# Kernel optimization log

Hardware: AMD Instinct MI355X
Metric: run time of the kernel (lower is better)

## Reference

```python
import jax, jax.numpy as jnp
import numpy as np
import math

DIM = 1024
N_HEADS = 16
HEAD_DIM = DIM // N_HEADS
MAX_LEN = 4096
THETA = 10000.0
LN_EPS = 1e-5


def _rope_tables(dim, max_len, theta=THETA):
    # matches precompute_rope: freqs over even indices, angles = outer(t, freqs)
    inv = 1.0 / theta ** (np.arange(0, dim, 2, dtype=np.float32) / dim)
    t = np.arange(max_len, dtype=np.float32)
    ang = np.outer(t, inv)  # [max_len, dim//2]
    return jnp.asarray(np.cos(ang)), jnp.asarray(np.sin(ang))


def setup_inputs() -> dict:
    key = jax.random.key(0)
    ks = jax.random.split(key, 5)
    B, T, D = 2, 2048, DIM
    s = 1.0 / math.sqrt(D)
    x = jax.random.normal(ks[0], (B, T, D), dtype=jnp.float32)
    wq = jax.random.normal(ks[1], (D, D), dtype=jnp.float32) * s
    wk = jax.random.normal(ks[2], (D, D), dtype=jnp.float32) * s
    wv = jax.random.normal(ks[3], (D, D), dtype=jnp.float32) * s
    wo = jax.random.normal(ks[4], (D, D), dtype=jnp.float32) * s
    ln_g = jnp.ones((D,), dtype=jnp.float32)
    ln_b = jnp.zeros((D,), dtype=jnp.float32)
    cos, sin = _rope_tables(HEAD_DIM, MAX_LEN)
    return {"x": x, "wq": wq, "wk": wk, "wv": wv, "wo": wo,
            "ln_g": ln_g, "ln_b": ln_b, "cos": cos, "sin": sin}


def _rotate(x, cos, sin):
    # x: [B, T, H, hd]; complex multiply on interleaved (even, odd) pairs
    B, T, H, hd = x.shape
    xr = x.reshape(B, T, H, hd // 2, 2)
    x0, x1 = xr[..., 0], xr[..., 1]
    c = cos[None, :T, None, :]
    s = sin[None, :T, None, :]
    o0 = x0 * c - x1 * s
    o1 = x0 * s + x1 * c
    return jnp.stack([o0, o1], axis=-1).reshape(B, T, H, hd)


def reference(x, wq, wk, wv, wo, ln_g, ln_b, cos, sin):
    B, T, D = x.shape
    H, hd = N_HEADS, HEAD_DIM
    # LayerNorm
    mu = jnp.mean(x, axis=-1, keepdims=True)
    var = jnp.var(x, axis=-1, keepdims=True)
    h = (x - mu) * jax.lax.rsqrt(var + LN_EPS) * ln_g + ln_b
    # QKV projections (torch Linear: h @ W.T)
    q = jnp.einsum('btd,ed->bte', h, wq).reshape(B, T, H, hd)
    k = jnp.einsum('btd,ed->bte', h, wk).reshape(B, T, H, hd)
    v = jnp.einsum('btd,ed->bte', h, wv).reshape(B, T, H, hd)
    q = _rotate(q, cos, sin)
    k = _rotate(k, cos, sin)
    # full (non-causal) attention, scores [B, H, T, T]
    scores = jnp.einsum('bqhd,bkhd->bhqk', q, k) / math.sqrt(hd)
    attn = jax.nn.softmax(scores, axis=-1)
    out = jnp.einsum('bhqk,bkhd->bqhd', attn, v).reshape(B, T, D)
    return jnp.einsum('btd,ed->bte', out, wo)
```

## Files before the change

kernel.cpp:

```cpp
#include <hip/hip_runtime.h>
#include <hip/hip_bf16.h>

typedef __attribute__((ext_vector_type(4))) float          fx4;
typedef __attribute__((ext_vector_type(8))) __bf16         bfx8;
typedef __attribute__((ext_vector_type(8))) unsigned short usx8;
typedef __attribute__((ext_vector_type(4))) unsigned short usx4;

#define TLEN 2048
#define ROWS 4096
#define D    1024

__device__ __forceinline__ float bf2f(unsigned short u) {
    union { unsigned int i; float f; } v; v.i = ((unsigned int)u) << 16; return v.f;
}
__device__ __forceinline__ unsigned short f2bf(float f) {
    union { float f; unsigned int i; } v; v.f = f;
    unsigned int r = v.i + 0x7fffu + ((v.i >> 16) & 1u);
    return (unsigned short)(r >> 16);
}
__device__ __forceinline__ unsigned int cvtpk_bf16(float lo, float hi) {
    unsigned int r;
    asm("v_cvt_pk_bf16_f32 %0, %1, %2" : "=v"(r) : "v"(lo), "v"(hi));
    return r;
}
__device__ __forceinline__ void gload_lds16(const unsigned short* g, unsigned short* l) {
    __builtin_amdgcn_global_load_lds((const __attribute__((address_space(1))) void*)g,
                                     (__attribute__((address_space(3))) void*)l, 16, 0, 0);
}

__device__ __forceinline__ usx4 cvt4(fx4 a) {
    usx4 o;
    #pragma unroll
    for (int j = 0; j < 4; j++) o[j] = f2bf(a[j]);
    return o;
}
__global__ __launch_bounds__(256) void prep_kernel(const float* __restrict__ x,
                                                   const float* __restrict__ g,
                                                   const float* __restrict__ bta,
                                                   const float* __restrict__ wq, const float* __restrict__ wk,
                                                   const float* __restrict__ wv, const float* __restrict__ wo,
                                                   unsigned short* __restrict__ hout,
                                                   unsigned short* __restrict__ wqkv,
                                                   unsigned short* __restrict__ wob,
                                                   float* __restrict__ ropeTab) {
    const int tid = threadIdx.x;
    if (blockIdx.x >= 5120) {
        const int idx = (blockIdx.x - 5120) * 256 + tid;
        const int pi_ = idx >> 11, t = idx & 2047;
        float inv = __builtin_amdgcn_exp2f(-0.415241011861f * (float)pi_);
        float ang = (float)t * inv;
        ropeTab[idx * 2]     = cosf(ang);
        ropeTab[idx * 2 + 1] = sinf(ang);
        return;
    }
    if (blockIdx.x >= 4096) {
        const int i = (blockIdx.x - 4096) * 256 + tid;
        ((usx4*)wqkv)[i]          = cvt4(((const fx4*)wq)[i]);
        ((usx4*)wqkv)[262144 + i] = cvt4(((const fx4*)wk)[i]);
        ((usx4*)wqkv)[524288 + i] = cvt4(((const fx4*)wv)[i]);
        ((usx4*)wob)[i]           = cvt4(((const fx4*)wo)[i]);
        return;
    }
    const int row = blockIdx.x;
    fx4 v = ((const fx4*)(x + (size_t)row * D))[tid];
    float s  = v[0] + v[1] + v[2] + v[3];
    float s2 = v[0]*v[0] + v[1]*v[1] + v[2]*v[2] + v[3]*v[3];
    #pragma unroll
    for (int mk = 32; mk >= 1; mk >>= 1) { s += __shfl_xor(s, mk); s2 += __shfl_xor(s2, mk); }
    __shared__ float red[8];
    const int wave = tid >> 6, lane = tid & 63;
    if (lane == 0) { red[wave] = s; red[4 + wave] = s2; }
    __syncthreads();
    s  = red[0] + red[1] + red[2] + red[3];
    s2 = red[4] + red[5] + red[6] + red[7];
    float mu   = s * (1.0f / D);
    float var  = s2 * (1.0f / D) - mu * mu;
    float rstd = rsqrtf(var + 1e-5f);
    fx4 gv = ((const fx4*)g)[tid];
    fx4 bv = ((const fx4*)bta)[tid];
    usx4 o;
    #pragma unroll
    for (int j = 0; j < 4; j++) o[j] = f2bf((v[j] - mu) * rstd * gv[j] + bv[j]);
    ((usx4*)hout)[(size_t)row * 256 + tid] = o;
}

__global__ __launch_bounds__(512) void qkvt_gemm(const unsigned short* __restrict__ hbuf,
                                                 const unsigned short* __restrict__ wqkv,
                                                 unsigned short* __restrict__ qkout,
                                                 unsigned short* __restrict__ vtout,
                                                 const float* __restrict__ ropeTab) {
    constexpr int K = 1024;
    __shared__ __align__(16) unsigned short As[2][256 * 64];
    __shared__ __align__(16) unsigned short Bs[2][256 * 64];
    const int tid = threadIdx.x, lane = tid & 63, wave = tid >> 6;
    const int fr = lane & 15, fq = lane >> 4;
    const int wr = wave >> 2, wc = wave & 3;

    const int id = blockIdx.x;
    const bool isqk = id < 128;
    int bm, bn;
    const unsigned short *Ab, *Bb;
    if (isqk) {
        bm = id & 15; bn = id >> 4;
        Ab = hbuf + (size_t)(bm * 256) * K;
        Bb = wqkv + (size_t)(bn * 256) * K;
    } else {
        int j = id - 128; bm = j & 3; bn = j >> 2;
        Ab = wqkv + (size_t)(2048 * 1024) + (size_t)(bm * 256) * K;
        Bb = hbuf + (size_t)(bn * 256) * K;
    }

    const int srow   = wave * 8 + (lane >> 3);
    const int sc_dst = (lane & 7) * 8;
    const int sc_src = ((lane & 7) ^ (lane >> 3)) * 8;

    #define STAGE_Q(BUF, KT)                                                          \
        {                                                                             \
            _Pragma("unroll")                                                         \
            for (int i = 0; i < 4; i++) {                                             \
                const int r = srow + 64 * i;                                          \
                gload_lds16(Ab + (size_t)r * K + (KT) + sc_src, &As[BUF][r * 64 + sc_dst]); \
                gload_lds16(Bb + (size_t)r * K + (KT) + sc_src, &Bs[BUF][r * 64 + sc_dst]); \
            }                                                                         \
        }

    fx4 acc[8][4];
    #pragma unroll
    for (int m = 0; m < 8; m++)
        #pragma unroll
        for (int n = 0; n < 4; n++) acc[m][n] = (fx4)0.0f;

    STAGE_Q(0, 0)

    for (int kt = 0; kt < K; kt += 64) {
        const int b = (kt >> 6) & 1;
        __syncthreads();
        if (kt + 64 < K) STAGE_Q(b ^ 1, kt + 64)
        #pragma unroll
        for (int s = 0; s < 2; s++) {
            bfx8 aF[8], bF[4];
            #pragma unroll
            for (int m = 0; m < 8; m++)
                aF[m] = *(const bfx8*)&As[b][(wr * 128 + m * 16 + fr) * 64 + (((s * 4 + fq) ^ (fr & 7)) * 8)];
            #pragma unroll
            for (int n = 0; n < 4; n++)
                bF[n] = *(const bfx8*)&Bs[b][(wc * 64 + n * 16 + fr) * 64 + (((s * 4 + fq) ^ (fr & 7)) * 8)];
            #pragma unroll
            for (int m = 0; m < 8; m++)
                #pragma unroll
                for (int n = 0; n < 4; n++)
                    acc[m][n] = __builtin_amdgcn_mfma_f32_16x16x32_bf16(aF[m], bF[n], acc[m][n], 0, 0, 0);
        }
    }
    #undef STAGE_Q

    const int row0 = bm * 256 + wr * 128 + fq * 4;
    const int col0 = bn * 256 + wc * 64 + fr;
    if (isqk) {
        const float QS = 0.125f * 1.44269504088896f;
        const bool isq = bn < 4;
        const float sgn = (fr & 1) ? 1.0f : -1.0f;
        #pragma unroll
        for (int m = 0; m < 8; m++) {
            const int rbase = row0 + m * 16;
            const int tb = rbase & (TLEN - 1);
            #pragma unroll
            for (int n = 0; n < 4; n++) {
                const float* tp = ropeTab + ((((n * 8 + (fr >> 1)) << 11) | tb) << 1);
                fx4 csA = *(const fx4*)tp;
                fx4 csB = *(const fx4*)(tp + 4);
                #pragma unroll
                for (int j = 0; j < 4; j++) {
                    float c  = (j < 2) ? csA[2 * j]     : csB[2 * (j - 2)];
                    float s_ = (j < 2) ? csA[2 * j + 1] : csB[2 * (j - 2) + 1];
                    float self = acc[m][n][j];
                    float other = __shfl_xor(self, 1);
                    float o = self * c + other * (sgn * s_);
                    if (isq) o *= QS;
                    qkout[(size_t)(rbase + j) * 2048 + col0 + n * 16] = f2bf(o);
                }
            }
        }
    } else {
        const int bb = bn >> 3;
        #pragma unroll
        for (int m = 0; m < 8; m++)
            #pragma unroll
            for (int n = 0; n < 4; n++) {
                const int t = (col0 + n * 16) & (TLEN - 1);
                const int tp = (t & ~63) | ((n >> 1) * 32 + ((fr >> 2)) * 8 + ((n & 1)) * 4 + (fr & 3));
                #pragma unroll
                for (int j = 0; j < 4; j++) {
                    const int d = row0 + m * 16 + j;
                    vtout[(((size_t)(bb * 16 + (d >> 6)) * 64) + (d & 63)) * TLEN + tp] = f2bf(acc[m][n][j]);
                }
            }
    }
}

__global__ __launch_bounds__(256) void gemm_out64(const unsigned short* __restrict__ A,
                                                  const unsigned short* __restrict__ B,
                                                  float* __restrict__ C) {
    constexpr int K = 1024;
    __shared__ __align__(16) unsigned short As[128 * 64];
    __shared__ __align__(16) unsigned short Bs[64 * 64];
    const int tid = threadIdx.x, lane = tid & 63, wave = tid >> 6;
    const int fr = lane & 15, fq = lane >> 4;
    const int bm = blockIdx.x, bn = blockIdx.y;
    const int wr = wave >> 1, wc = wave & 1;

    const int srow   = wave * 8 + (lane >> 3);
    const int sc_dst = (lane & 7) * 8;
    const int sc_src = ((lane & 7) ^ (lane >> 3)) * 8;
    const unsigned short* Ab = A + (size_t)(bm * 128) * K;
    const unsigned short* Bb = B + (size_t)(bn * 64) * K;

    fx4 acc[4][2];
    #pragma unroll
    for (int m = 0; m < 4; m++)
        #pragma unroll
        for (int n = 0; n < 2; n++) acc[m][n] = (fx4)0.0f;

    for (int kt = 0; kt < K; kt += 64) {
        #pragma unroll
        for (int i = 0; i < 4; i++) {
            const int r = srow + 32 * i;
            gload_lds16(Ab + (size_t)r * K + kt + sc_src, &As[r * 64 + sc_dst]);
            if (i < 2)
                gload_lds16(Bb + (size_t)r * K + kt + sc_src, &Bs[r * 64 + sc_dst]);
        }
        __syncthreads();
        #pragma unroll
        for (int s = 0; s < 2; s++) {
            bfx8 aF[4], bF[2];
            #pragma unroll
            for (int m = 0; m < 4; m++)
                aF[m] = *(const bfx8*)&As[(wr * 64 + m * 16 + fr) * 64 + (((s * 4 + fq) ^ (fr & 7)) * 8)];
            #pragma unroll
            for (int n = 0; n < 2; n++)
                bF[n] = *(const bfx8*)&Bs[(wc * 32 + n * 16 + fr) * 64 + (((s * 4 + fq) ^ (fr & 7)) * 8)];
            #pragma unroll
            for (int m = 0; m < 4; m++)
                #pragma unroll
                for (int n = 0; n < 2; n++)
                    acc[m][n] = __builtin_amdgcn_mfma_f32_16x16x32_bf16(aF[m], bF[n], acc[m][n], 0, 0, 0);
        }
        __syncthreads();
    }

    const int row0 = bm * 128 + wr * 64 + fq * 4;
    const int col0 = bn * 64 + wc * 32 + fr;
    #pragma unroll
    for (int m = 0; m < 4; m++)
        #pragma unroll
        for (int n = 0; n < 2; n++)
            #pragma unroll
            for (int j = 0; j < 4; j++)
                C[(size_t)(row0 + m * 16 + j) * 1024 + col0 + n * 16] = acc[m][n][j];
}

__global__ __launch_bounds__(512) void attn_kernel(const unsigned short* __restrict__ qk,
                                                   const unsigned short* __restrict__ vt,
                                                   unsigned short* __restrict__ ao) {
    const int flat = blockIdx.x + (blockIdx.y << 3);
    const int sid  = (flat & 7) * 32 + (flat >> 3);
    const int qt = sid & 7, bh = sid >> 3;
    const int b = bh >> 4, hh = bh & 15;
    const int tid = threadIdx.x, lane = tid & 63, wave = tid >> 6;
    const int fr = lane & 15, fq = lane >> 4;

    __shared__ __align__(16) unsigned short sK[2][128 * 64];
    __shared__ __align__(16) unsigned short sVt[2][2 * 64 * 64];

    const size_t rs = 2048;
    const unsigned short* qb  = qk + (size_t)b * TLEN * rs + hh * 64;
    const unsigned short* kb  = qb + 1024;
    const unsigned short* vtb = vt + (size_t)bh * (64 * TLEN);

    bfx8 qF[2][2];
    #pragma unroll
    for (int g = 0; g < 2; g++) {
        int qrow = qt * 256 + wave * 32 + g * 16 + fr;
        const unsigned short* qp = qb + (size_t)qrow * rs + fq * 8;
        qF[g][0] = *(const bfx8*)qp;
        qF[g][1] = *(const bfx8*)(qp + 32);
    }
    union { unsigned short us[8]; bfx8 bf; } ones_u;
    #pragma unroll
    for (int i = 0; i < 8; i++) ones_u.us[i] = 0x3F80;

    const int srow = lane >> 3;
    const int scol = ((lane & 7) ^ srow) * 8;

    #define STAGE_ATTN(BUF, KT)                                                          \
        {                                                                                \
            _Pragma("unroll")                                                            \
            for (int i = 0; i < 2; i++) {                                                \
                const int rg = wave * 2 + i;                                             \
                gload_lds16(kb + (size_t)((KT) + rg * 8 + srow) * rs + scol,             \
                            &sK[BUF][rg * 512 + lane * 8]);                              \
                const int sub = rg >> 3, drow = (rg & 7) * 8 + srow;                     \
                gload_lds16(vtb + (size_t)drow * TLEN + (KT) + sub * 64 + scol,          \
                            &sVt[BUF][rg * 512 + lane * 8]);                             \
            }                                                                            \
        }

    STAGE_ATTN(0, 0)

    fx4 oacc[2][4];
    fx4 oextra[2] = {(fx4)0.0f, (fx4)0.0f};
    #pragma unroll
    for (int g = 0; g < 2; g++)
        #pragma unroll
        for (int db = 0; db < 4; db++) oacc[g][db] = (fx4)0.0f;

    #pragma unroll 2
    for (int t = 0; t < 16; ++t) {
        const int buf = t & 1;
        __syncthreads();

        if (t + 1 < 16) STAGE_ATTN(buf ^ 1, (t + 1) * 128)

        fx4 s0[8], s1[8];
        #pragma unroll
        for (int n = 0; n < 8; n++) { s0[n] = (fx4)0.0f; s1[n] = (fx4)0.0f; }
        __builtin_amdgcn_s_setprio(1);
        #pragma unroll
        for (int s = 0; s < 2; s++)
            #pragma unroll
            for (int n = 0; n < 8; n++) {
                bfx8 kF = *(const bfx8*)&sK[buf][(n * 16 + fr) * 64 + (((s * 4 + fq) ^ (fr & 7)) * 8)];
                s0[n] = __builtin_amdgcn_mfma_f32_16x16x32_bf16(kF, qF[0][s], s0[n], 0, 0, 0);
                s1[n] = __builtin_amdgcn_mfma_f32_16x16x32_bf16(kF, qF[1][s], s1[n], 0, 0, 0);
            }
        __builtin_amdgcn_s_setprio(0);

        unsigned int u0[8][2], u1[8][2];
        #pragma unroll
        for (int n = 0; n < 8; n++) {
            u0[n][0] = cvtpk_bf16(__builtin_amdgcn_exp2f(s0[n][0]), __builtin_amdgcn_exp2f(s0[n][1]));
            u0[n][1] = cvtpk_bf16(__builtin_amdgcn_exp2f(s0[n][2]), __builtin_amdgcn_exp2f(s0[n][3]));
        }

        __builtin_amdgcn_s_setprio(1);
        #pragma unroll
        for (int sp = 0; sp < 4; sp++) {
            union { unsigned int ui[4]; bfx8 bf; } cv;
            cv.ui[0] = u0[2 * sp][0];     cv.ui[1] = u0[2 * sp][1];
            cv.ui[2] = u0[2 * sp + 1][0]; cv.ui[3] = u0[2 * sp + 1][1];
            #pragma unroll
            for (int db = 0; db < 4; db++) {
                bfx8 vF = *(const bfx8*)&sVt[buf][(sp >> 1) * 4096 + (db * 16 + fr) * 64 +
                                                 ((((sp & 1) * 4 + fq) ^ (fr & 7)) * 8)];
                oacc[0][db] = __builtin_amdgcn_mfma_f32_16x16x32_bf16(vF, cv.bf, oacc[0][db], 0, 0, 0);
            }
            oextra[0] = __builtin_amdgcn_mfma_f32_16x16x32_bf16(ones_u.bf, cv.bf, oextra[0], 0, 0, 0);
        }
        __builtin_amdgcn_s_setprio(0);

        #pragma unroll
        for (int n = 0; n < 8; n++) {
            u1[n][0] = cvtpk_bf16(__builtin_amdgcn_exp2f(s1[n][0]), __builtin_amdgcn_exp2f(s1[n][1]));
            u1[n][1] = cvtpk_bf16(__builtin_amdgcn_exp2f(s1[n][2]), __builtin_amdgcn_exp2f(s1[n][3]));
        }

        __builtin_amdgcn_s_setprio(1);
        #pragma unroll
        for (int sp = 0; sp < 4; sp++) {
            union { unsigned int ui[4]; bfx8 bf; } cv;
            cv.ui[0] = u1[2 * sp][0];     cv.ui[1] = u1[2 * sp][1];
            cv.ui[2] = u1[2 * sp + 1][0]; cv.ui[3] = u1[2 * sp + 1][1];
            #pragma unroll
            for (int db = 0; db < 4; db++) {
                bfx8 vF = *(const bfx8*)&sVt[buf][(sp >> 1) * 4096 + (db * 16 + fr) * 64 +
                                                 ((((sp & 1) * 4 + fq) ^ (fr & 7)) * 8)];
                oacc[1][db] = __builtin_amdgcn_mfma_f32_16x16x32_bf16(vF, cv.bf, oacc[1][db], 0, 0, 0);
            }
            oextra[1] = __builtin_amdgcn_mfma_f32_16x16x32_bf16(ones_u.bf, cv.bf, oextra[1], 0, 0, 0);
        }
        __builtin_amdgcn_s_setprio(0);
    }
    #undef STAGE_ATTN

    #pragma unroll
    for (int g = 0; g < 2; g++) {
        float invl = 1.0f / oextra[g][0];
        const int qrow = qt * 256 + wave * 32 + g * 16 + fr;
        unsigned short* aop = ao + (size_t)(b * TLEN + qrow) * 1024 + hh * 64 + fq * 4;
        #pragma unroll
        for (int db = 0; db < 4; db++) {
            usx4 o4;
            #pragma unroll
            for (int j = 0; j < 4; j++) o4[j] = f2bf(oacc[g][db][j] * invl);
            *(usx4*)(aop + db * 16) = o4;
        }
    }
}

extern "C" void kernel_launch(void* const* d_in, const int* in_sizes, int n_in,
                              void* d_out, int out_size, void* d_ws, size_t ws_size,
                              hipStream_t stream) {
    const float* x    = (const float*)d_in[0];
    const float* wq   = (const float*)d_in[1];
    const float* wk   = (const float*)d_in[2];
    const float* wv   = (const float*)d_in[3];
    const float* wo   = (const float*)d_in[4];
    const float* lng  = (const float*)d_in[5];
    const float* lnb  = (const float*)d_in[6];

    char* ws = (char*)d_ws;
    unsigned short* wob  = (unsigned short*)(ws);
    unsigned short* wqkv = (unsigned short*)(ws + (2u  << 20));
    unsigned short* hbuf = (unsigned short*)(ws + (8u  << 20));
    unsigned short* qk   = (unsigned short*)(ws + (16u << 20));
    unsigned short* vtb  = (unsigned short*)(ws + (32u << 20));
    unsigned short* ao   = (unsigned short*)(ws + (8u  << 20));
    float* ropeTab = (float*)d_out;

    prep_kernel<<<5632, 256, 0, stream>>>(x, lng, lnb, wq, wk, wv, wo, hbuf, wqkv, wob, ropeTab);
    qkvt_gemm<<<192, 512, 0, stream>>>(hbuf, wqkv, qk, vtb, ropeTab);
    attn_kernel<<<dim3(8, 32), 512, 0, stream>>>(qk, vtb, ao);
    gemm_out64<<<dim3(32, 16), 256, 0, stream>>>(ao, wob, (float*)d_out);
}
```

Baseline: 108.4 us.

## Split QKV GEMM into smaller tiles with more blocks, drop double buffering

The QKV projection GEMM goes from 192 blocks of 512 threads with 256x256 double-buffered tiles to 512 blocks of 256 threads. QK uses 128x256 tiles and V^T uses 128x128 tiles, both with a single LDS buffer and two barriers per k-step. The aim is to fill all 256 CUs of the MI355X (192 blocks left many idle) and allow more resident blocks per CU. In exchange the in-kernel load/compute overlap from double buffering is lost, and data reuse per tile is lower.

```diff
diff --git a/kernel.cpp b/kernel.cpp
--- a/kernel.cpp
+++ b/kernel.cpp
@@ -84,79 +84,66 @@
     ((usx4*)hout)[(size_t)row * 256 + tid] = o;
 }
 
-__global__ __launch_bounds__(512) void qkvt_gemm(const unsigned short* __restrict__ hbuf,
+__global__ __launch_bounds__(256) void qkvt_gemm(const unsigned short* __restrict__ hbuf,
                                                  const unsigned short* __restrict__ wqkv,
                                                  unsigned short* __restrict__ qkout,
                                                  unsigned short* __restrict__ vtout,
                                                  const float* __restrict__ ropeTab) {
     constexpr int K = 1024;
-    __shared__ __align__(16) unsigned short As[2][256 * 64];
-    __shared__ __align__(16) unsigned short Bs[2][256 * 64];
+    __shared__ __align__(16) unsigned short As[128 * 64];
+    __shared__ __align__(16) unsigned short Bs[256 * 64];
     const int tid = threadIdx.x, lane = tid & 63, wave = tid >> 6;
     const int fr = lane & 15, fq = lane >> 4;
-    const int wr = wave >> 2, wc = wave & 3;
-
-    const int id = blockIdx.x;
-    const bool isqk = id < 128;
-    int bm, bn;
-    const unsigned short *Ab, *Bb;
-    if (isqk) {
-        bm = id & 15; bn = id >> 4;
-        Ab = hbuf + (size_t)(bm * 256) * K;
-        Bb = wqkv + (size_t)(bn * 256) * K;
-    } else {
-        int j = id - 128; bm = j & 3; bn = j >> 2;
-        Ab = wqkv + (size_t)(2048 * 1024) + (size_t)(bm * 256) * K;
-        Bb = hbuf + (size_t)(bn * 256) * K;
-    }
 
     const int srow   = wave * 8 + (lane >> 3);
     const int sc_dst = (lane & 7) * 8;
     const int sc_src = ((lane & 7) ^ (lane >> 3)) * 8;
 
-    #define STAGE_Q(BUF, KT)                                                          \
-        {                                                                             \
-            _Pragma("unroll")                                                         \
-            for (int i = 0; i < 4; i++) {                                             \
-                const int r = srow + 64 * i;                                          \
-                gload_lds16(Ab + (size_t)r * K + (KT) + sc_src, &As[BUF][r * 64 + sc_dst]); \
-                gload_lds16(Bb + (size_t)r * K + (KT) + sc_src, &Bs[BUF][r * 64 + sc_dst]); \
-            }                                                                         \
-        }
-
-    fx4 acc[8][4];
-    #pragma unroll
-    for (int m = 0; m < 8; m++)
-        #pragma unroll
-        for (int n = 0; n < 4; n++) acc[m][n] = (fx4)0.0f;
-
-    STAGE_Q(0, 0)
-
-    for (int kt = 0; kt < K; kt += 64) {
-        const int b = (kt >> 6) & 1;
-        __syncthreads();
-        if (kt + 64 < K) STAGE_Q(b ^ 1, kt + 64)
-        #pragma unroll
-        for (int s = 0; s < 2; s++) {
-            bfx8 aF[8], bF[4];
-            #pragma unroll
-            for (int m = 0; m < 8; m++)
-                aF[m] = *(const bfx8*)&As[b][(wr * 128 + m * 16 + fr) * 64 + (((s * 4 + fq) ^ (fr & 7)) * 8)];
-            #pragma unroll
-            for (int n = 0; n < 4; n++)
-                bF[n] = *(const bfx8*)&Bs[b][(wc * 64 + n * 16 + fr) * 64 + (((s * 4 + fq) ^ (fr & 7)) * 8)];
-            #pragma unroll
-            for (int m = 0; m < 8; m++)
+    const int id = blockIdx.x;
+    if (id < 256) {
+        const int bm = id & 31, bn = id >> 5;
+        const unsigned short* Ab = hbuf + (size_t)(bm * 128) * K;
+        const unsigned short* Bb = wqkv + (size_t)(bn * 256) * K;
+        const int wc = wave;
+
+        fx4 acc[8][4];
+        #pragma unroll
+        for (int m = 0; m < 8; m++)
+            #pragma unroll
+            for (int n = 0; n < 4; n++) acc[m][n] = (fx4)0.0f;
+
+        for (int kt = 0; kt < K; kt += 64) {
+            #pragma unroll
+            for (int i = 0; i < 4; i++) {
+                const int r = srow + 32 * i;
+                gload_lds16(Ab + (size_t)r * K + kt + sc_src, &As[r * 64 + sc_dst]);
+            }
+            #pragma unroll
+            for (int i = 0; i < 8; i++) {
+                const int r = srow + 32 * i;
+                gload_lds16(Bb + (size_t)r * K + kt + sc_src, &Bs[r * 64 + sc_dst]);
+            }
+            __syncthreads();
+            #pragma unroll
+            for (int s = 0; s < 2; s++) {
+                bfx8 aF[8], bF[4];
+                #pragma unroll
+                for (int m = 0; m < 8; m++)
+                    aF[m] = *(const bfx8*)&As[(m * 16 + fr) * 64 + (((s * 4 + fq) ^ (fr & 7)) * 8)];
                 #pragma unroll
                 for (int n = 0; n < 4; n++)
-                    acc[m][n] = __builtin_amdgcn_mfma_f32_16x16x32_bf16(aF[m], bF[n], acc[m][n], 0, 0, 0);
-        }
-    }
-    #undef STAGE_Q
-
-    const int row0 = bm * 256 + wr * 128 + fq * 4;
-    const int col0 = bn * 256 + wc * 64 + fr;
-    if (isqk) {
+                    bF[n] = *(const bfx8*)&Bs[(wc * 64 + n * 16 + fr) * 64 + (((s * 4 + fq) ^ (fr & 7)) * 8)];
+                #pragma unroll
+                for (int m = 0; m < 8; m++)
+                    #pragma unroll
+                    for (int n = 0; n < 4; n++)
+                        acc[m][n] = __builtin_amdgcn_mfma_f32_16x16x32_bf16(aF[m], bF[n], acc[m][n], 0, 0, 0);
+            }
+            __syncthreads();
+        }
+
+        const int row0 = bm * 128 + fq * 4;
+        const int col0 = bn * 256 + wc * 64 + fr;
         const float QS = 0.125f * 1.44269504088896f;
         const bool isq = bn < 4;
         const float sgn = (fr & 1) ? 1.0f : -1.0f;
@@ -182,9 +169,49 @@
             }
         }
     } else {
-        const int bb = bn >> 3;
-        #pragma unroll
-        for (int m = 0; m < 8; m++)
+        const int j2 = id - 256;
+        const int bm = j2 & 7, bn = j2 >> 3;
+        const unsigned short* Ab = wqkv + (size_t)(2048 * 1024) + (size_t)(bm * 128) * K;
+        const unsigned short* Bb = hbuf + (size_t)(bn * 128) * K;
+        const int wr = wave >> 1, wc = wave & 1;
+
+        fx4 acc[4][4];
+        #pragma unroll
+        for (int m = 0; m < 4; m++)
+            #pragma unroll
+            for (int n = 0; n < 4; n++) acc[m][n] = (fx4)0.0f;
+
+        for (int kt = 0; kt < K; kt += 64) {
+            #pragma unroll
+            for (int i = 0; i < 4; i++) {
+                const int r = srow + 32 * i;
+                gload_lds16(Ab + (size_t)r * K + kt + sc_src, &As[r * 64 + sc_dst]);
+                gload_lds16(Bb + (size_t)r * K + kt + sc_src, &Bs[r * 64 + sc_dst]);
+            }
+            __syncthreads();
+            #pragma unroll
+            for (int s = 0; s < 2; s++) {
+                bfx8 aF[4], bF[4];
+                #pragma unroll
+                for (int m = 0; m < 4; m++)
+                    aF[m] = *(const bfx8*)&As[(wr * 64 + m * 16 + fr) * 64 + (((s * 4 + fq) ^ (fr & 7)) * 8)];
+                #pragma unroll
+                for (int n = 0; n < 4; n++)
+                    bF[n] = *(const bfx8*)&Bs[(wc * 64 + n * 16 + fr) * 64 + (((s * 4 + fq) ^ (fr & 7)) * 8)];
+                #pragma unroll
+                for (int m = 0; m < 4; m++)
+                    #pragma unroll
+                    for (int n = 0; n < 4; n++)
+                        acc[m][n] = __builtin_amdgcn_mfma_f32_16x16x32_bf16(aF[m], bF[n], acc[m][n], 0, 0, 0);
+            }
+            __syncthreads();
+        }
+
+        const int row0 = bm * 128 + wr * 64 + fq * 4;
+        const int col0 = bn * 128 + wc * 64 + fr;
+        const int bb = bn >> 4;
+        #pragma unroll
+        for (int m = 0; m < 4; m++)
             #pragma unroll
             for (int n = 0; n < 4; n++) {
                 const int t = (col0 + n * 16) & (TLEN - 1);
@@ -418,7 +445,7 @@
     float* ropeTab = (float*)d_out;
 
     prep_kernel<<<5632, 256, 0, stream>>>(x, lng, lnb, wq, wk, wv, wo, hbuf, wqkv, wob, ropeTab);
-    qkvt_gemm<<<192, 512, 0, stream>>>(hbuf, wqkv, qk, vtb, ropeTab);
+    qkvt_gemm<<<512, 256, 0, stream>>>(hbuf, wqkv, qk, vtb, ropeTab);
     attn_kernel<<<dim3(8, 32), 512, 0, stream>>>(qk, vtb, ao);
     gemm_out64<<<dim3(32, 16), 256, 0, stream>>>(ao, wob, (float*)d_out);
 }
```

New measurement: 119.9 us. 10.6% more time.
